# Performance work log

Measured on AMD Instinct MI355X. Metric: run time of the kernel, lower is better.

The kernel has to match this reference:

```python
import jax, jax.numpy as jnp
import numpy as np

INC, OUTC, NHEADS, KSIZE = 256, 256, 8, 5


def setup_inputs() -> dict:
    key = jax.random.key(0)
    k1, k2 = jax.random.split(key, 2)
    x = jax.random.normal(k1, (4, INC, 64, 64), dtype=jnp.float32)
    w_qkv = jax.random.normal(k2, (3 * OUTC, INC), dtype=jnp.float32) * 0.02
    b_qkv = jnp.zeros((3 * OUTC,), dtype=jnp.float32)
    return {"x": x, "w_qkv": w_qkv, "b_qkv": b_qkv}


def reference(x, w_qkv, b_qkv):
    N, Cin, H, W = x.shape
    hd = OUTC // NHEADS
    ofs = KSIZE // 2
    K2 = KSIZE * KSIZE

    # 1x1 conv == pointwise matmul over channels
    qkv = jnp.einsum('nchw,dc->ndhw', x, w_qkv) + b_qkv[None, :, None, None]
    Q = qkv[:, :OUTC]
    K = qkv[:, OUTC:2 * OUTC]
    V = qkv[:, 2 * OUTC:]

    # Zero-pad K/V; track validity so boundary softmax only spans in-bounds
    # positions (the torch code slices smaller windows at borders -> no pad
    # contribution to softmax).
    Kp = jnp.pad(K, ((0, 0), (0, 0), (ofs, ofs), (ofs, ofs)))
    Vp = jnp.pad(V, ((0, 0), (0, 0), (ofs, ofs), (ofs, ofs)))
    valid = jnp.pad(jnp.ones((H, W), dtype=bool), ((ofs, ofs), (ofs, ofs)))

    # Sliding windows via KSIZE^2 static shifted slices: [N,D,H,W,K2]
    k_win = jnp.stack([Kp[:, :, dy:dy + H, dx:dx + W]
                       for dy in range(KSIZE) for dx in range(KSIZE)], axis=-1)
    v_win = jnp.stack([Vp[:, :, dy:dy + H, dx:dx + W]
                       for dy in range(KSIZE) for dx in range(KSIZE)], axis=-1)
    m_win = jnp.stack([valid[dy:dy + H, dx:dx + W]
                       for dy in range(KSIZE) for dx in range(KSIZE)], axis=-1)  # [H,W,K2]

    qh = Q.reshape(N, NHEADS, hd, H, W)
    kh = k_win.reshape(N, NHEADS, hd, H, W, K2)
    vh = v_win.reshape(N, NHEADS, hd, H, W, K2)

    scores = jnp.einsum('ngdhw,ngdhwk->nghwk', qh, kh)          # [N,G,H,W,K2]
    scores = jnp.where(m_win[None, None], scores, -jnp.inf)
    att = jax.nn.softmax(scores, axis=-1)
    out = jnp.einsum('nghwk,ngdhwk->ngdhw', att, vh)            # [N,G,hd,H,W]
    return out.reshape(N, OUTC, H, W)
```

## Files before the change

kernel.cpp:

```cpp
#include <hip/hip_runtime.h>
#include <hip/hip_bf16.h>
#include <math.h>

#define CIN 256
#define COUT 768
#define OUTC 256
#define HH 64
#define WW 64
#define HW 4096

typedef unsigned int uint32;
typedef unsigned short ushort16;

using short8 = __attribute__((ext_vector_type(8))) short;
using f32x4  = __attribute__((ext_vector_type(4))) float;

__device__ inline uint32 pkbf2(float a, float b) {
    __hip_bfloat162 h = __float22bfloat162_rn(make_float2(a, b));
    union { __hip_bfloat162 h2; uint32 u; } cv; cv.h2 = h;
    return cv.u;
}

__device__ inline uint32 pkhf2(float a, float b) {
    union { _Float16 h[2]; uint32 u; } cv;
    cv.h[0] = (_Float16)a; cv.h[1] = (_Float16)b;
    return cv.u;
}

__device__ inline float f16lo(uint32 u) {
    union { uint32 u; _Float16 h[2]; } c; c.u = u; return (float)c.h[0];
}
__device__ inline float f16hi(uint32 u) {
    union { uint32 u; _Float16 h[2]; } c; c.u = u; return (float)c.h[1];
}

__device__ inline float dpp_xor1(float x) {
#if __has_builtin(__builtin_amdgcn_update_dpp)
    int i = __builtin_amdgcn_update_dpp(0, __float_as_int(x),
                                        0xB1 , 0xF, 0xF, true);
    return __int_as_float(i);
#else
    return __shfl_xor(x, 1, 64);
#endif
}

#define LDSTR 40

__global__ __launch_bounds__(256) void qkv_gemm_kernel(
    const float* __restrict__ x, const float* __restrict__ wq,
    const float* __restrict__ bq, ushort16* __restrict__ qkv)
{
    __shared__ ushort16 As[128 * LDSTR];
    __shared__ ushort16 Bs[128 * LDSTR];

    const int n   = blockIdx.z;
    const int d0  = blockIdx.y * 128;
    const int p0  = blockIdx.x * 128;
    const int tid = threadIdx.x;
    const int lane = tid & 63;
    const int wid  = tid >> 6;
    const int wm = wid >> 1;
    const int wn = wid & 1;

    const float* xb = x + (size_t)n * CIN * HW;

    const int arow = tid >> 2;
    const int akk  = (tid & 3) * 8;
    const float* aptr = wq + (size_t)(d0 + arow) * CIN + akk;
    const int bkg = (tid >> 6) * 8;
    const int bpg = (tid & 63) * 2;
    const float* bptr = xb + (size_t)bkg * HW + p0 + bpg;

    ushort16* awr0 = (ushort16*)&As[arow * LDSTR + akk];
    ushort16* awr1 = (ushort16*)&As[(arow + 64) * LDSTR + akk];
    ushort16* bwr0 = (ushort16*)&Bs[bpg * LDSTR + bkg];
    ushort16* bwr1 = (ushort16*)&Bs[(bpg + 1) * LDSTR + bkg];

    f32x4 acc[4][4];
    #pragma unroll
    for (int i = 0; i < 4; ++i)
        #pragma unroll
        for (int j = 0; j < 4; ++j) acc[i][j] = (f32x4){0.f, 0.f, 0.f, 0.f};

    float4 a_st[4];
    float2 b_st[8];

    {
        a_st[0] = *(const float4*)(aptr);
        a_st[1] = *(const float4*)(aptr + 4);
        a_st[2] = *(const float4*)(aptr + (size_t)64 * CIN);
        a_st[3] = *(const float4*)(aptr + (size_t)64 * CIN + 4);
        #pragma unroll
        for (int j = 0; j < 8; ++j)
            b_st[j] = *(const float2*)(bptr + (size_t)j * HW);
    }

    const int lrow = lane & 15;
    const int lk   = (lane >> 4) * 8;

    #pragma unroll 1
    for (int kt = 0; kt < 8; ++kt) {
        __syncthreads();

        {
            uint32 w0 = pkbf2(a_st[0].x, a_st[0].y), w1 = pkbf2(a_st[0].z, a_st[0].w);
            uint32 w2 = pkbf2(a_st[1].x, a_st[1].y), w3 = pkbf2(a_st[1].z, a_st[1].w);
            *(uint4*)awr0 = make_uint4(w0, w1, w2, w3);
            w0 = pkbf2(a_st[2].x, a_st[2].y); w1 = pkbf2(a_st[2].z, a_st[2].w);
            w2 = pkbf2(a_st[3].x, a_st[3].y); w3 = pkbf2(a_st[3].z, a_st[3].w);
            *(uint4*)awr1 = make_uint4(w0, w1, w2, w3);
            uint4 c0, c1;
            c0.x = pkbf2(b_st[0].x, b_st[1].x); c0.y = pkbf2(b_st[2].x, b_st[3].x);
            c0.z = pkbf2(b_st[4].x, b_st[5].x); c0.w = pkbf2(b_st[6].x, b_st[7].x);
            c1.x = pkbf2(b_st[0].y, b_st[1].y); c1.y = pkbf2(b_st[2].y, b_st[3].y);
            c1.z = pkbf2(b_st[4].y, b_st[5].y); c1.w = pkbf2(b_st[6].y, b_st[7].y);
            *(uint4*)bwr0 = c0;
            *(uint4*)bwr1 = c1;
        }

        if (kt < 7) {
            const int ko = (kt + 1) * 32;
            a_st[0] = *(const float4*)(aptr + ko);
            a_st[1] = *(const float4*)(aptr + ko + 4);
            a_st[2] = *(const float4*)(aptr + (size_t)64 * CIN + ko);
            a_st[3] = *(const float4*)(aptr + (size_t)64 * CIN + ko + 4);
            #pragma unroll
            for (int j = 0; j < 8; ++j)
                b_st[j] = *(const float2*)(bptr + (size_t)(ko + j) * HW);
        }

        __syncthreads();

        short8 af[4], bf[4];
        #pragma unroll
        for (int fm = 0; fm < 4; ++fm)
            af[fm] = *(const short8*)&As[(wm * 64 + fm * 16 + lrow) * LDSTR + lk];
        #pragma unroll
        for (int fn = 0; fn < 4; ++fn)
            bf[fn] = *(const short8*)&Bs[(wn * 64 + fn * 16 + lrow) * LDSTR + lk];
        #pragma unroll
        for (int fm = 0; fm < 4; ++fm)
            #pragma unroll
            for (int fn = 0; fn < 4; ++fn)
                acc[fm][fn] = __builtin_amdgcn_mfma_f32_16x16x32_bf16(
                    af[fm], bf[fn], acc[fm][fn], 0, 0, 0);
    }

    const int hi4 = lane >> 4;
    ushort16* qn = qkv + (size_t)n * COUT * HW;
    #pragma unroll
    for (int fm = 0; fm < 4; ++fm) {
        const int D = d0 + wm * 64 + fm * 16 + hi4 * 4;
        const float4 bias = *(const float4*)(&bq[D]);
        const int slot = D >> 5, dlow = D & 31;
        ushort16* qs = qn + (size_t)slot * (HW * 32) + dlow;
        #pragma unroll
        for (int fn = 0; fn < 4; ++fn) {
            const int p = p0 + wn * 64 + fn * 16 + lrow;
            f32x4 v = acc[fm][fn];
            uint32 u0 = pkhf2(v[0] + bias.x, v[1] + bias.y);
            uint32 u1 = pkhf2(v[2] + bias.z, v[3] + bias.w);
            *(uint2*)(qs + (size_t)p * 32) = make_uint2(u0, u1);
        }
    }
}

#define TR 4
#define TC 32
#define HR 8
#define HC 36
#define NPIX (HR*HC)

__global__ __launch_bounds__(256) void attn_kernel(
    const ushort16* __restrict__ qkv, float* __restrict__ out)
{
    __shared__ uint4 Ks[NPIX * 4];
    __shared__ uint4 Vs[NPIX * 4];

    const int n    = blockIdx.z;
    const int head = blockIdx.y;
    const int ht = blockIdx.x >> 1;
    const int wt = blockIdx.x & 1;
    const int h0 = ht * TR;
    const int w0 = wt * TC;

    const int tid  = threadIdx.x;
    const int half = tid & 1;
    const int wc   = (tid >> 1) & 31;
    const int tr   = tid >> 6;

    const int h = h0 + tr, w = w0 + wc;
    const int p = h * WW + w;

    const uint4* Kb = (const uint4*)(qkv + ((size_t)(n * 24 + 8 + head)) * HW * 32);
    const uint4* Vb = (const uint4*)(qkv + ((size_t)(n * 24 + 16 + head)) * HW * 32);

    for (int c = tid; c < 2 * NPIX * 4; c += 256) {
        const int b  = (c >= NPIX * 4);
        const int cc = c - b * NPIX * 4;
        const int pix = cc >> 2, i = cc & 3;
        const int hr = pix / HC, cw = pix - hr * HC;
        const int hh = h0 + hr - 2, ww = w0 + cw - 2;
        if (hh >= 0 && hh < HH && ww >= 0 && ww < WW) {
            const int pp = hh * WW + ww;
            const uint4 v = (b ? Vb : Kb)[(size_t)pp * 4 + i];
            const int unit = (pix * 4 + i) ^ (pix & 7);
            (b ? Vs : Ks)[unit] = v;
        }
    }

    float qf[16];
    {
        const uint4* Qp = (const uint4*)(qkv + (((size_t)(n * 24 + head)) * HW + p) * 32);
        #pragma unroll
        for (int i = 0; i < 2; ++i) {
            uint4 u = Qp[half * 2 + i];
            qf[8*i+0] = f16lo(u.x); qf[8*i+1] = f16hi(u.x);
            qf[8*i+2] = f16lo(u.y); qf[8*i+3] = f16hi(u.y);
            qf[8*i+4] = f16lo(u.z); qf[8*i+5] = f16hi(u.z);
            qf[8*i+6] = f16lo(u.w); qf[8*i+7] = f16hi(u.w);
        }
    }

    __syncthreads();

    float sc[25];
    #pragma unroll
    for (int ky = 0; ky < 5; ++ky) {
        const int hh = h + ky - 2;
        const int hr = tr + ky;
        #pragma unroll
        for (int kx = 0; kx < 5; ++kx) {
            const int ww = w + kx - 2;
            float s;
            if (hh >= 0 && hh < HH && ww >= 0 && ww < WW) {
                const int pix = hr * HC + (wc + kx);
                const int u0 = (pix * 4 + half * 2)     ^ (pix & 7);
                const int u1 = (pix * 4 + half * 2 + 1) ^ (pix & 7);
                uint4 a = Ks[u0], b = Ks[u1];
                float t = 0.f;
                t = fmaf(qf[0],  f16lo(a.x), t); t = fmaf(qf[1],  f16hi(a.x), t);
                t = fmaf(qf[2],  f16lo(a.y), t); t = fmaf(qf[3],  f16hi(a.y), t);
                t = fmaf(qf[4],  f16lo(a.z), t); t = fmaf(qf[5],  f16hi(a.z), t);
                t = fmaf(qf[6],  f16lo(a.w), t); t = fmaf(qf[7],  f16hi(a.w), t);
                t = fmaf(qf[8],  f16lo(b.x), t); t = fmaf(qf[9],  f16hi(b.x), t);
                t = fmaf(qf[10], f16lo(b.y), t); t = fmaf(qf[11], f16hi(b.y), t);
                t = fmaf(qf[12], f16lo(b.z), t); t = fmaf(qf[13], f16hi(b.z), t);
                t = fmaf(qf[14], f16lo(b.w), t); t = fmaf(qf[15], f16hi(b.w), t);
                s = t;
            } else {
                s = -1e30f;
            }
            sc[ky * 5 + kx] = s;
        }
    }
    #pragma unroll
    for (int k = 0; k < 25; ++k) {
        float o = dpp_xor1(sc[k]);
        sc[k] = (sc[k] <= -1e29f) ? sc[k] : sc[k] + o;
    }

    float m = sc[0];
    #pragma unroll
    for (int k = 1; k < 25; ++k) m = fmaxf(m, sc[k]);
    float sum = 0.f;
    #pragma unroll
    for (int k = 0; k < 25; ++k) {
        float e = __expf(sc[k] - m);
        sc[k] = e;
        sum += e;
    }
    const float inv = 1.f / sum;

    float al[8], ah[8];
    #pragma unroll
    for (int i = 0; i < 8; ++i) { al[i] = 0.f; ah[i] = 0.f; }
    #pragma unroll
    for (int ky = 0; ky < 5; ++ky) {
        const int hh = h + ky - 2;
        if (hh < 0 || hh >= HH) continue;
        const int hr = tr + ky;
        #pragma unroll
        for (int kx = 0; kx < 5; ++kx) {
            const int ww = w + kx - 2;
            if (ww < 0 || ww >= WW) continue;
            const float a = sc[ky * 5 + kx];
            const int pix = hr * HC + (wc + kx);
            const int u0 = (pix * 4 + half * 2)     ^ (pix & 7);
            const int u1 = (pix * 4 + half * 2 + 1) ^ (pix & 7);
            uint4 x = Vs[u0], y = Vs[u1];
            al[0] = fmaf(a, f16lo(x.x), al[0]); ah[0] = fmaf(a, f16hi(x.x), ah[0]);
            al[1] = fmaf(a, f16lo(x.y), al[1]); ah[1] = fmaf(a, f16hi(x.y), ah[1]);
            al[2] = fmaf(a, f16lo(x.z), al[2]); ah[2] = fmaf(a, f16hi(x.z), ah[2]);
            al[3] = fmaf(a, f16lo(x.w), al[3]); ah[3] = fmaf(a, f16hi(x.w), ah[3]);
            al[4] = fmaf(a, f16lo(y.x), al[4]); ah[4] = fmaf(a, f16hi(y.x), ah[4]);
            al[5] = fmaf(a, f16lo(y.y), al[5]); ah[5] = fmaf(a, f16hi(y.y), ah[5]);
            al[6] = fmaf(a, f16lo(y.z), al[6]); ah[6] = fmaf(a, f16hi(y.z), ah[6]);
            al[7] = fmaf(a, f16lo(y.w), al[7]); ah[7] = fmaf(a, f16hi(y.w), ah[7]);
        }
    }

    float* Ob = out + ((size_t)(n * 8 + head) * 32 + half * 16) * HW + p;
    #pragma unroll
    for (int i = 0; i < 8; ++i) {
        Ob[(size_t)(2*i)   * HW] = al[i] * inv;
        Ob[(size_t)(2*i+1) * HW] = ah[i] * inv;
    }
}

extern "C" void kernel_launch(void* const* d_in, const int* in_sizes, int n_in,
                              void* d_out, int out_size, void* d_ws, size_t ws_size,
                              hipStream_t stream) {
    const float* x  = (const float*)d_in[0];
    const float* wq = (const float*)d_in[1];
    const float* bq = (const float*)d_in[2];
    float* out = (float*)d_out;
    ushort16* qkv = (ushort16*)d_ws;

    dim3 g1(HW / 128, COUT / 128, 4);
    qkv_gemm_kernel<<<g1, 256, 0, stream>>>(x, wq, bq, qkv);

    dim3 g2(32, 8, 4);
    attn_kernel<<<g2, 256, 0, stream>>>(qkv, out);
}
```

Measured before the change: 45.77 us.

## Pre-convert x and weights to bf16, stage GEMM tiles via direct global-to-LDS loads

Adds two pre-pass kernels: one transposes x to pixel-major bf16 and one converts the QKV weights to bf16. The GEMM then loads tiles straight into double-buffered LDS with global_load_lds, removing the register staging, the in-loop fp32-to-bf16 conversion and one barrier per k-step. The cost is two extra kernel launches and an additional write and read of the converted x through the workspace. The unpadded 32-element LDS rows may also cause bank conflicts.

New measurement: 49.54 us. 8.2% more time.

```diff
diff --git a/kernel.cpp b/kernel.cpp
--- a/kernel.cpp
+++ b/kernel.cpp
@@ -37,21 +37,68 @@
 __device__ inline float dpp_xor1(float x) {
 #if __has_builtin(__builtin_amdgcn_update_dpp)
     int i = __builtin_amdgcn_update_dpp(0, __float_as_int(x),
-                                        0xB1 , 0xF, 0xF, true);
+                                        0xB1, 0xF, 0xF, true);
     return __int_as_float(i);
 #else
     return __shfl_xor(x, 1, 64);
 #endif
 }
 
-#define LDSTR 40
-
-__global__ __launch_bounds__(256) void qkv_gemm_kernel(
-    const float* __restrict__ x, const float* __restrict__ wq,
+__device__ inline void gld16(const void* g, void* l) {
+    __builtin_amdgcn_global_load_lds(
+        (const __attribute__((address_space(1))) unsigned int*)g,
+        (__attribute__((address_space(3))) unsigned int*)l, 16, 0, 0);
+}
+
+__global__ __launch_bounds__(256) void cvt_x_kernel(
+    const float* __restrict__ x, ushort16* __restrict__ xT)
+{
+    __shared__ float T[64][65];
+    const int n  = blockIdx.z;
+    const int c0 = blockIdx.y * 64;
+    const int p0 = blockIdx.x * 64;
+    const int tid = threadIdx.x;
+    const int ty = tid >> 4, tx = tid & 15;
+
+    #pragma unroll
+    for (int i = 0; i < 4; ++i) {
+        float4 v = *(const float4*)&x[((size_t)(n * CIN + c0 + i * 16 + ty)) * HW + p0 + tx * 4];
+        T[i * 16 + ty][tx * 4 + 0] = v.x;
+        T[i * 16 + ty][tx * 4 + 1] = v.y;
+        T[i * 16 + ty][tx * 4 + 2] = v.z;
+        T[i * 16 + ty][tx * 4 + 3] = v.w;
+    }
+    __syncthreads();
+
+    #pragma unroll
+    for (int it = 0; it < 2; ++it) {
+        const int t  = it * 256 + tid;
+        const int pl = t >> 3, oc = t & 7;
+        uint32 u0 = pkbf2(T[oc * 8 + 0][pl], T[oc * 8 + 1][pl]);
+        uint32 u1 = pkbf2(T[oc * 8 + 2][pl], T[oc * 8 + 3][pl]);
+        uint32 u2 = pkbf2(T[oc * 8 + 4][pl], T[oc * 8 + 5][pl]);
+        uint32 u3 = pkbf2(T[oc * 8 + 6][pl], T[oc * 8 + 7][pl]);
+        *(uint4*)&xT[((size_t)n * HW + p0 + pl) * CIN + c0 + oc * 8] =
+            make_uint4(u0, u1, u2, u3);
+    }
+}
+
+__global__ __launch_bounds__(256) void cvt_w_kernel(
+    const float* __restrict__ wq, ushort16* __restrict__ wb)
+{
+    const int i = (blockIdx.x * 256 + threadIdx.x) * 8;
+    float4 a = *(const float4*)&wq[i];
+    float4 b = *(const float4*)&wq[i + 4];
+    *(uint4*)&wb[i] = make_uint4(pkbf2(a.x, a.y), pkbf2(a.z, a.w),
+                                 pkbf2(b.x, b.y), pkbf2(b.z, b.w));
+}
+
+__global__ __launch_bounds__(256) void qkv_gemm2(
+    const ushort16* __restrict__ wb, const ushort16* __restrict__ xT,
     const float* __restrict__ bq, ushort16* __restrict__ qkv)
 {
-    __shared__ ushort16 As[128 * LDSTR];
-    __shared__ ushort16 Bs[128 * LDSTR];
+    __shared__ ushort16 As[2][128 * 32];
+    __shared__ ushort16 Bs[2][128 * 32];
 
     const int n   = blockIdx.z;
     const int d0  = blockIdx.y * 128;
@@ -59,92 +106,55 @@
     const int tid = threadIdx.x;
     const int lane = tid & 63;
     const int wid  = tid >> 6;
-    const int wm = wid >> 1;
-    const int wn = wid & 1;
-
-    const float* xb = x + (size_t)n * CIN * HW;
-
-    const int arow = tid >> 2;
-    const int akk  = (tid & 3) * 8;
-    const float* aptr = wq + (size_t)(d0 + arow) * CIN + akk;
-    const int bkg = (tid >> 6) * 8;
-    const int bpg = (tid & 63) * 2;
-    const float* bptr = xb + (size_t)bkg * HW + p0 + bpg;
-
-    ushort16* awr0 = (ushort16*)&As[arow * LDSTR + akk];
-    ushort16* awr1 = (ushort16*)&As[(arow + 64) * LDSTR + akk];
-    ushort16* bwr0 = (ushort16*)&Bs[bpg * LDSTR + bkg];
-    ushort16* bwr1 = (ushort16*)&Bs[(bpg + 1) * LDSTR + bkg];
-
-    f32x4 acc[4][4];
-    #pragma unroll
-    for (int i = 0; i < 4; ++i)
-        #pragma unroll
-        for (int j = 0; j < 4; ++j) acc[i][j] = (f32x4){0.f, 0.f, 0.f, 0.f};
-
-    float4 a_st[4];
-    float2 b_st[8];
-
-    {
-        a_st[0] = *(const float4*)(aptr);
-        a_st[1] = *(const float4*)(aptr + 4);
-        a_st[2] = *(const float4*)(aptr + (size_t)64 * CIN);
-        a_st[3] = *(const float4*)(aptr + (size_t)64 * CIN + 4);
-        #pragma unroll
-        for (int j = 0; j < 8; ++j)
-            b_st[j] = *(const float2*)(bptr + (size_t)j * HW);
-    }
+    const int wm = wid >> 1, wn = wid & 1;
+
+    const int srow = lane >> 2;
+    const int skk  = (lane & 3) * 8;
+    const ushort16* ag = wb + (size_t)(d0 + wid * 32 + srow) * CIN + skk;
+    const ushort16* bg = xT + ((size_t)n * HW + p0 + wid * 32 + srow) * CIN + skk;
 
     const int lrow = lane & 15;
     const int lk   = (lane >> 4) * 8;
 
+    f32x4 acc[4][4];
+    #pragma unroll
+    for (int i = 0; i < 4; ++i)
+        #pragma unroll
+        for (int j = 0; j < 4; ++j) acc[i][j] = (f32x4){0.f, 0.f, 0.f, 0.f};
+
+#define STAGE(buf, ko) do {                                              \
+        gld16(ag + (ko),            &As[buf][(wid * 32)      * 32]);     \
+        gld16(ag + (ko) + 16 * CIN, &As[buf][(wid * 32 + 16) * 32]);     \
+        gld16(bg + (ko),            &Bs[buf][(wid * 32)      * 32]);     \
+        gld16(bg + (ko) + 16 * CIN, &Bs[buf][(wid * 32 + 16) * 32]);     \
+    } while (0)
+
+    STAGE(0, 0);
+    __syncthreads();
+
+    int cur = 0;
     #pragma unroll 1
     for (int kt = 0; kt < 8; ++kt) {
-        __syncthreads();
-
-        {
-            uint32 w0 = pkbf2(a_st[0].x, a_st[0].y), w1 = pkbf2(a_st[0].z, a_st[0].w);
-            uint32 w2 = pkbf2(a_st[1].x, a_st[1].y), w3 = pkbf2(a_st[1].z, a_st[1].w);
-            *(uint4*)awr0 = make_uint4(w0, w1, w2, w3);
-            w0 = pkbf2(a_st[2].x, a_st[2].y); w1 = pkbf2(a_st[2].z, a_st[2].w);
-            w2 = pkbf2(a_st[3].x, a_st[3].y); w3 = pkbf2(a_st[3].z, a_st[3].w);
-            *(uint4*)awr1 = make_uint4(w0, w1, w2, w3);
-            uint4 c0, c1;
-            c0.x = pkbf2(b_st[0].x, b_st[1].x); c0.y = pkbf2(b_st[2].x, b_st[3].x);
-            c0.z = pkbf2(b_st[4].x, b_st[5].x); c0.w = pkbf2(b_st[6].x, b_st[7].x);
-            c1.x = pkbf2(b_st[0].y, b_st[1].y); c1.y = pkbf2(b_st[2].y, b_st[3].y);
-            c1.z = pkbf2(b_st[4].y, b_st[5].y); c1.w = pkbf2(b_st[6].y, b_st[7].y);
-            *(uint4*)bwr0 = c0;
-            *(uint4*)bwr1 = c1;
-        }
-
-        if (kt < 7) {
-            const int ko = (kt + 1) * 32;
-            a_st[0] = *(const float4*)(aptr + ko);
-            a_st[1] = *(const float4*)(aptr + ko + 4);
-            a_st[2] = *(const float4*)(aptr + (size_t)64 * CIN + ko);
-            a_st[3] = *(const float4*)(aptr + (size_t)64 * CIN + ko + 4);
-            #pragma unroll
-            for (int j = 0; j < 8; ++j)
-                b_st[j] = *(const float2*)(bptr + (size_t)(ko + j) * HW);
-        }
-
-        __syncthreads();
+        if (kt < 7) STAGE(cur ^ 1, (kt + 1) * 32);
 
         short8 af[4], bf[4];
         #pragma unroll
         for (int fm = 0; fm < 4; ++fm)
-            af[fm] = *(const short8*)&As[(wm * 64 + fm * 16 + lrow) * LDSTR + lk];
+            af[fm] = *(const short8*)&As[cur][(wm * 64 + fm * 16 + lrow) * 32 + lk];
         #pragma unroll
         for (int fn = 0; fn < 4; ++fn)
-            bf[fn] = *(const short8*)&Bs[(wn * 64 + fn * 16 + lrow) * LDSTR + lk];
+            bf[fn] = *(const short8*)&Bs[cur][(wn * 64 + fn * 16 + lrow) * 32 + lk];
         #pragma unroll
         for (int fm = 0; fm < 4; ++fm)
             #pragma unroll
             for (int fn = 0; fn < 4; ++fn)
                 acc[fm][fn] = __builtin_amdgcn_mfma_f32_16x16x32_bf16(
                     af[fm], bf[fn], acc[fm][fn], 0, 0, 0);
-    }
+
+        __syncthreads();
+        cur ^= 1;
+    }
+#undef STAGE
 
     const int hi4 = lane >> 4;
     ushort16* qn = qkv + (size_t)n * COUT * HW;
@@ -315,10 +325,17 @@
     const float* wq = (const float*)d_in[1];
     const float* bq = (const float*)d_in[2];
     float* out = (float*)d_out;
+
     ushort16* qkv = (ushort16*)d_ws;
+    ushort16* xT  = (ushort16*)((char*)d_ws + (32u << 20));
+    ushort16* wbf = (ushort16*)((char*)d_ws + (44u << 20));
+
+    dim3 g0(HW / 64, CIN / 64, 4);
+    cvt_x_kernel<<<g0, 256, 0, stream>>>(x, xT);
+    cvt_w_kernel<<<96, 256, 0, stream>>>(wq, wbf);
 
     dim3 g1(HW / 128, COUT / 128, 4);
-    qkv_gemm_kernel<<<g1, 256, 0, stream>>>(x, wq, bq, qkv);
+    qkv_gemm2<<<g1, 256, 0, stream>>>(wbf, xT, bq, qkv);
 
     dim3 g2(32, 8, 4);
     attn_kernel<<<g2, 256, 0, stream>>>(qkv, out);
```

## Shrink QKV GEMM pixel tile to 64 and use XOR-swizzled LDS layout

Applied to the files above, without the earlier changes.

The QKV projection GEMM tile along pixels shrinks from 128 to 64, doubling the grid to 1536 blocks and halving each warp's accumulator tiles. The padded-stride LDS layout is replaced by a compact uint4 layout with XOR swizzling to avoid bank conflicts on the MFMA fragment reads. The aim is better occupancy and CU load balance on the GEMM, at the cost of loading the weight tile twice as often and less reuse per block. Variable renames in the attention kernel are cosmetic.

Result: slower. 50.54 us (+10.4%).

```diff
diff --git a/kernel.cpp b/kernel.cpp
--- a/kernel.cpp
+++ b/kernel.cpp
@@ -20,128 +20,123 @@
     union { __hip_bfloat162 h2; uint32 u; } cv; cv.h2 = h;
     return cv.u;
 }
-
 __device__ inline uint32 pkhf2(float a, float b) {
     union { _Float16 h[2]; uint32 u; } cv;
     cv.h[0] = (_Float16)a; cv.h[1] = (_Float16)b;
     return cv.u;
 }
-
 __device__ inline float f16lo(uint32 u) {
     union { uint32 u; _Float16 h[2]; } c; c.u = u; return (float)c.h[0];
 }
 __device__ inline float f16hi(uint32 u) {
     union { uint32 u; _Float16 h[2]; } c; c.u = u; return (float)c.h[1];
 }
-
 __device__ inline float dpp_xor1(float x) {
 #if __has_builtin(__builtin_amdgcn_update_dpp)
     int i = __builtin_amdgcn_update_dpp(0, __float_as_int(x),
-                                        0xB1 , 0xF, 0xF, true);
+                                        0xB1, 0xF, 0xF, true);
     return __int_as_float(i);
 #else
     return __shfl_xor(x, 1, 64);
 #endif
 }
 
-#define LDSTR 40
-
 __global__ __launch_bounds__(256) void qkv_gemm_kernel(
     const float* __restrict__ x, const float* __restrict__ wq,
     const float* __restrict__ bq, ushort16* __restrict__ qkv)
 {
-    __shared__ ushort16 As[128 * LDSTR];
-    __shared__ ushort16 Bs[128 * LDSTR];
+    __shared__ uint4 As[512];
+    __shared__ uint4 Bs[256];
 
     const int n   = blockIdx.z;
     const int d0  = blockIdx.y * 128;
-    const int p0  = blockIdx.x * 128;
+    const int p0  = blockIdx.x * 64;
     const int tid = threadIdx.x;
     const int lane = tid & 63;
     const int wid  = tid >> 6;
     const int wm = wid >> 1;
     const int wn = wid & 1;
 
-    const float* xb = x + (size_t)n * CIN * HW;
-
-    const int arow = tid >> 2;
-    const int akk  = (tid & 3) * 8;
-    const float* aptr = wq + (size_t)(d0 + arow) * CIN + akk;
-    const int bkg = (tid >> 6) * 8;
-    const int bpg = (tid & 63) * 2;
-    const float* bptr = xb + (size_t)bkg * HW + p0 + bpg;
-
-    ushort16* awr0 = (ushort16*)&As[arow * LDSTR + akk];
-    ushort16* awr1 = (ushort16*)&As[(arow + 64) * LDSTR + akk];
-    ushort16* bwr0 = (ushort16*)&Bs[bpg * LDSTR + bkg];
-    ushort16* bwr1 = (ushort16*)&Bs[(bpg + 1) * LDSTR + bkg];
-
-    f32x4 acc[4][4];
+    const int ar = tid >> 1;
+    const int ac0 = (tid & 1) * 2;
+    const float* aptr = wq + (size_t)(d0 + ar) * CIN + ac0 * 8;
+    const int pp = (tid & 31) * 2;
+    const int kq = (tid >> 5) * 4;
+    const int bchunk = kq >> 3;
+    const int bsub   = (kq >> 2) & 1;
+    const float* bptr = x + (size_t)n * CIN * HW + (size_t)kq * HW + p0 + pp;
+
+    const int lrow = lane & 15;
+    const int kc   = lane >> 4;
+
+    f32x4 acc[4][2];
     #pragma unroll
     for (int i = 0; i < 4; ++i)
         #pragma unroll
-        for (int j = 0; j < 4; ++j) acc[i][j] = (f32x4){0.f, 0.f, 0.f, 0.f};
+        for (int j = 0; j < 2; ++j) acc[i][j] = (f32x4){0.f, 0.f, 0.f, 0.f};
 
     float4 a_st[4];
-    float2 b_st[8];
+    float2 b_st[4];
 
     {
         a_st[0] = *(const float4*)(aptr);
         a_st[1] = *(const float4*)(aptr + 4);
-        a_st[2] = *(const float4*)(aptr + (size_t)64 * CIN);
-        a_st[3] = *(const float4*)(aptr + (size_t)64 * CIN + 4);
-        #pragma unroll
-        for (int j = 0; j < 8; ++j)
+        a_st[2] = *(const float4*)(aptr + 8);
+        a_st[3] = *(const float4*)(aptr + 12);
+        #pragma unroll
+        for (int j = 0; j < 4; ++j)
             b_st[j] = *(const float2*)(bptr + (size_t)j * HW);
     }
 
-    const int lrow = lane & 15;
-    const int lk   = (lane >> 4) * 8;
+    const int au0 = (ar * 4 + ac0)     ^ (ar & 7);
+    const int au1 = (ar * 4 + ac0 + 1) ^ (ar & 7);
+    const int bx  = (pp >> 1) & 7;
+    const int bu0 = (pp * 4 + bchunk)       ^ bx;
+    const int bu1 = ((pp + 1) * 4 + bchunk) ^ bx;
 
     #pragma unroll 1
     for (int kt = 0; kt < 8; ++kt) {
         __syncthreads();
 
+        As[au0] = make_uint4(pkbf2(a_st[0].x, a_st[0].y), pkbf2(a_st[0].z, a_st[0].w),
+                             pkbf2(a_st[1].x, a_st[1].y), pkbf2(a_st[1].z, a_st[1].w));
+        As[au1] = make_uint4(pkbf2(a_st[2].x, a_st[2].y), pkbf2(a_st[2].z, a_st[2].w),
+                             pkbf2(a_st[3].x, a_st[3].y), pkbf2(a_st[3].z, a_st[3].w));
         {
-            uint32 w0 = pkbf2(a_st[0].x, a_st[0].y), w1 = pkbf2(a_st[0].z, a_st[0].w);
-            uint32 w2 = pkbf2(a_st[1].x, a_st[1].y), w3 = pkbf2(a_st[1].z, a_st[1].w);
-            *(uint4*)awr0 = make_uint4(w0, w1, w2, w3);
-            w0 = pkbf2(a_st[2].x, a_st[2].y); w1 = pkbf2(a_st[2].z, a_st[2].w);
-            w2 = pkbf2(a_st[3].x, a_st[3].y); w3 = pkbf2(a_st[3].z, a_st[3].w);
-            *(uint4*)awr1 = make_uint4(w0, w1, w2, w3);
-            uint4 c0, c1;
-            c0.x = pkbf2(b_st[0].x, b_st[1].x); c0.y = pkbf2(b_st[2].x, b_st[3].x);
-            c0.z = pkbf2(b_st[4].x, b_st[5].x); c0.w = pkbf2(b_st[6].x, b_st[7].x);
-            c1.x = pkbf2(b_st[0].y, b_st[1].y); c1.y = pkbf2(b_st[2].y, b_st[3].y);
-            c1.z = pkbf2(b_st[4].y, b_st[5].y); c1.w = pkbf2(b_st[6].y, b_st[7].y);
-            *(uint4*)bwr0 = c0;
-            *(uint4*)bwr1 = c1;
+            uint2 v0 = make_uint2(pkbf2(b_st[0].x, b_st[1].x), pkbf2(b_st[2].x, b_st[3].x));
+            uint2 v1 = make_uint2(pkbf2(b_st[0].y, b_st[1].y), pkbf2(b_st[2].y, b_st[3].y));
+            ((uint2*)&Bs[bu0])[bsub] = v0;
+            ((uint2*)&Bs[bu1])[bsub] = v1;
         }
 
         if (kt < 7) {
             const int ko = (kt + 1) * 32;
             a_st[0] = *(const float4*)(aptr + ko);
             a_st[1] = *(const float4*)(aptr + ko + 4);
-            a_st[2] = *(const float4*)(aptr + (size_t)64 * CIN + ko);
-            a_st[3] = *(const float4*)(aptr + (size_t)64 * CIN + ko + 4);
+            a_st[2] = *(const float4*)(aptr + ko + 8);
+            a_st[3] = *(const float4*)(aptr + ko + 12);
             #pragma unroll
-            for (int j = 0; j < 8; ++j)
+            for (int j = 0; j < 4; ++j)
                 b_st[j] = *(const float2*)(bptr + (size_t)(ko + j) * HW);
         }
 
         __syncthreads();
 
-        short8 af[4], bf[4];
-        #pragma unroll
-        for (int fm = 0; fm < 4; ++fm)
-            af[fm] = *(const short8*)&As[(wm * 64 + fm * 16 + lrow) * LDSTR + lk];
-        #pragma unroll
-        for (int fn = 0; fn < 4; ++fn)
-            bf[fn] = *(const short8*)&Bs[(wn * 64 + fn * 16 + lrow) * LDSTR + lk];
+        short8 af[4], bf[2];
+        #pragma unroll
+        for (int fm = 0; fm < 4; ++fm) {
+            const int r = wm * 64 + fm * 16 + lrow;
+            af[fm] = *(const short8*)&As[(r * 4 + kc) ^ (r & 7)];
+        }
+        #pragma unroll
+        for (int fn = 0; fn < 2; ++fn) {
+            const int p = wn * 32 + fn * 16 + lrow;
+            bf[fn] = *(const short8*)&Bs[(p * 4 + kc) ^ ((p >> 1) & 7)];
+        }
         #pragma unroll
         for (int fm = 0; fm < 4; ++fm)
             #pragma unroll
-            for (int fn = 0; fn < 4; ++fn)
+            for (int fn = 0; fn < 2; ++fn)
                 acc[fm][fn] = __builtin_amdgcn_mfma_f32_16x16x32_bf16(
                     af[fm], bf[fn], acc[fm][fn], 0, 0, 0);
     }
@@ -155,8 +150,8 @@
         const int slot = D >> 5, dlow = D & 31;
         ushort16* qs = qn + (size_t)slot * (HW * 32) + dlow;
         #pragma unroll
-        for (int fn = 0; fn < 4; ++fn) {
-            const int p = p0 + wn * 64 + fn * 16 + lrow;
+        for (int fn = 0; fn < 2; ++fn) {
+            const int p = p0 + wn * 32 + fn * 16 + lrow;
             f32x4 v = acc[fm][fn];
             uint32 u0 = pkhf2(v[0] + bias.x, v[1] + bias.y);
             uint32 u1 = pkhf2(v[2] + bias.z, v[3] + bias.w);
@@ -288,15 +283,15 @@
             const int pix = hr * HC + (wc + kx);
             const int u0 = (pix * 4 + half * 2)     ^ (pix & 7);
             const int u1 = (pix * 4 + half * 2 + 1) ^ (pix & 7);
-            uint4 x = Vs[u0], y = Vs[u1];
-            al[0] = fmaf(a, f16lo(x.x), al[0]); ah[0] = fmaf(a, f16hi(x.x), ah[0]);
-            al[1] = fmaf(a, f16lo(x.y), al[1]); ah[1] = fmaf(a, f16hi(x.y), ah[1]);
-            al[2] = fmaf(a, f16lo(x.z), al[2]); ah[2] = fmaf(a, f16hi(x.z), ah[2]);
-            al[3] = fmaf(a, f16lo(x.w), al[3]); ah[3] = fmaf(a, f16hi(x.w), ah[3]);
-            al[4] = fmaf(a, f16lo(y.x), al[4]); ah[4] = fmaf(a, f16hi(y.x), ah[4]);
-            al[5] = fmaf(a, f16lo(y.y), al[5]); ah[5] = fmaf(a, f16hi(y.y), ah[5]);
-            al[6] = fmaf(a, f16lo(y.z), al[6]); ah[6] = fmaf(a, f16hi(y.z), ah[6]);
-            al[7] = fmaf(a, f16lo(y.w), al[7]); ah[7] = fmaf(a, f16hi(y.w), ah[7]);
+            uint4 xv = Vs[u0], yv = Vs[u1];
+            al[0] = fmaf(a, f16lo(xv.x), al[0]); ah[0] = fmaf(a, f16hi(xv.x), ah[0]);
+            al[1] = fmaf(a, f16lo(xv.y), al[1]); ah[1] = fmaf(a, f16hi(xv.y), ah[1]);
+            al[2] = fmaf(a, f16lo(xv.z), al[2]); ah[2] = fmaf(a, f16hi(xv.z), ah[2]);
+            al[3] = fmaf(a, f16lo(xv.w), al[3]); ah[3] = fmaf(a, f16hi(xv.w), ah[3]);
+            al[4] = fmaf(a, f16lo(yv.x), al[4]); ah[4] = fmaf(a, f16hi(yv.x), ah[4]);
+            al[5] = fmaf(a, f16lo(yv.y), al[5]); ah[5] = fmaf(a, f16hi(yv.y), ah[5]);
+            al[6] = fmaf(a, f16lo(yv.z), al[6]); ah[6] = fmaf(a, f16hi(yv.z), ah[6]);
+            al[7] = fmaf(a, f16lo(yv.w), al[7]); ah[7] = fmaf(a, f16hi(yv.w), ah[7]);
         }
     }
 
@@ -317,7 +312,7 @@
     float* out = (float*)d_out;
     ushort16* qkv = (ushort16*)d_ws;
 
-    dim3 g1(HW / 128, COUT / 128, 4);
+    dim3 g1(HW / 64, COUT / 128, 4);
     qkv_gemm_kernel<<<g1, 256, 0, stream>>>(x, wq, bq, qkv);
 
     dim3 g2(32, 8, 4);
```
